# Performance work log

Measured on AMD Instinct MI355X. Metric: run time of the kernel, lower is better.

The kernel has to match this reference:

```python
import jax, jax.numpy as jnp
import numpy as np

DIM = 512
HEADS = 16
WIN = (8, 8)
N = WIN[0] * WIN[1]  # 64 tokens per window
BW = 1024            # batch * num_windows
TABLE = (2 * WIN[0] - 1) * (2 * WIN[1] - 1)  # 225


def _relative_position_index():
    ch, cw = np.arange(WIN[0]), np.arange(WIN[1])
    coords = np.stack(np.meshgrid(ch, cw, indexing='ij'))        # [2,Wh,Ww]
    flat = coords.reshape(2, -1)                                  # [2,N]
    rel = flat[:, :, None] - flat[:, None, :]                     # [2,N,N]
    rel = rel.transpose(1, 2, 0).astype(np.int64)                 # [N,N,2]
    rel[:, :, 0] += WIN[0] - 1
    rel[:, :, 1] += WIN[1] - 1
    rel[:, :, 0] *= 2 * WIN[1] - 1
    return jnp.asarray(rel.sum(-1), dtype=jnp.int32)              # [N,N]


def setup_inputs() -> dict:
    key = jax.random.key(0)
    ks = jax.random.split(key, 8)
    s = 0.02
    return {
        'q': jax.random.normal(ks[0], (BW, N, DIM), jnp.float32),
        'wq': jax.random.normal(ks[1], (DIM, DIM), jnp.float32) * s,
        'bq': jnp.zeros((DIM,), jnp.float32),
        'wkv': jax.random.normal(ks[2], (DIM, 2 * DIM), jnp.float32) * s,
        'bkv': jnp.zeros((2 * DIM,), jnp.float32),
        'wproj': jax.random.normal(ks[3], (DIM, DIM), jnp.float32) * s,
        'bproj': jnp.zeros((DIM,), jnp.float32),
        'bias_table': jax.random.normal(ks[4], (TABLE, HEADS), jnp.float32) * s,
        'rel_pos_index': _relative_position_index(),
    }


def reference(q, wq, bq, wkv, bkv, wproj, bproj, bias_table, rel_pos_index):
    B, n, C = q.shape
    hd = C // HEADS
    scale = hd ** -0.5
    # projections (torch Linear with pre-transposed weights)
    qh = (q @ wq + bq).reshape(B, n, HEADS, hd).transpose(0, 2, 1, 3) * scale  # [B,H,N,hd]
    kv = (q @ wkv + bkv).reshape(B, n, 2, HEADS, hd)
    k = kv[:, :, 0].transpose(0, 2, 1, 3)  # [B,H,N,hd]
    v = kv[:, :, 1].transpose(0, 2, 1, 3)
    attn = jnp.einsum('bhqd,bhkd->bhqk', qh, k)                   # [B,H,N,N]
    bias = bias_table[rel_pos_index].transpose(2, 0, 1)           # [H,N,N]
    attn = jax.nn.softmax(attn + bias[None], axis=-1)
    x = jnp.einsum('bhqk,bhkd->bqhd', attn, v).reshape(B, n, C)
    x = x @ wproj + bproj
    return x, attn
```

## Files before the change

kernel.cpp:

```cpp
#include <hip/hip_runtime.h>
#include <hip/hip_bf16.h>
#include <stdint.h>

typedef __attribute__((ext_vector_type(8))) __bf16 bf16x8;
typedef __attribute__((ext_vector_type(4))) float f32x4;

#define MFMA16(a, b, c) __builtin_amdgcn_mfma_f32_16x16x32_bf16(a, b, c, 0, 0, 0)

__device__ __forceinline__ void gload16(const void* g, void* l) {
  __builtin_amdgcn_global_load_lds((const __attribute__((address_space(1))) void*)g,
                                   (__attribute__((address_space(3))) void*)l, 16, 0, 0);
}

__global__ __launch_bounds__(256) void prep_kernel(
    const float* __restrict__ wq, const float* __restrict__ bq,
    const float* __restrict__ wkv, const float* __restrict__ bkv,
    const float* __restrict__ wproj, const float* __restrict__ btab,
    const int* __restrict__ relidx,
    __bf16* __restrict__ W1t, __bf16* __restrict__ WpT,
    float* __restrict__ bias1, float* __restrict__ bias_frag) {
  const float scale = 0.17677669529663687f;
  int t = blockIdx.x * 256 + threadIdx.x;
  if (t < 786432) {
    int j = t >> 9, kk = t & 511;
    float v = (j < 512) ? wq[kk * 512 + j] * scale : wkv[kk * 1024 + (j - 512)];
    W1t[t] = (__bf16)v;
  } else if (t < 1048576) {
    int u = t - 786432;
    int j = u >> 9, kk = u & 511;
    WpT[u] = (__bf16)wproj[kk * 512 + j];
  } else if (t < 1050112) {
    int j = t - 1048576;
    bias1[j] = (j < 512) ? bq[j] * scale : bkv[j - 512];
  } else if (t < 1115648) {
    int u = t - 1050112;
    int r = u & 3, l = (u >> 2) & 63, nj = (u >> 8) & 3, mi = (u >> 10) & 3, h = u >> 12;
    int qq = mi * 16 + (l >> 4) * 4 + r;
    int nn = nj * 16 + (l & 15);
    bias_frag[u] = btab[relidx[qq * 64 + nn] * 16 + h];
  }
}

__global__ __launch_bounds__(256) void cvt_kernel(const float* __restrict__ in,
                                                  __bf16* __restrict__ out) {
  int t = blockIdx.x * 256 + threadIdx.x;
  const float4* p = (const float4*)in + (size_t)t * 2;
  float4 a = p[0], b = p[1];
  bf16x8 v = {(__bf16)a.x, (__bf16)a.y, (__bf16)a.z, (__bf16)a.w,
              (__bf16)b.x, (__bf16)b.y, (__bf16)b.z, (__bf16)b.w};
  *((bf16x8*)out + t) = v;
}

__global__ __launch_bounds__(256) void gemm1_kernel(
    const __bf16* __restrict__ A, const __bf16* __restrict__ W1t,
    const float* __restrict__ bias1,
    __bf16* __restrict__ qh, __bf16* __restrict__ kb, __bf16* __restrict__ vv) {
  __shared__ __bf16 As[128 * 32];
  __shared__ __bf16 Bs[128 * 32];
  int tid = threadIdx.x;
  int w = tid >> 6, l = tid & 63, c = l & 15, g = l >> 4;
  int wm = w >> 1, wn = w & 1;
  int bflat = (blockIdx.x & 7) * 768 + (blockIdx.x >> 3);
  int bx = bflat % 12, by = bflat / 12;
  int r0 = by * 128, n0 = bx * 128;

  f32x4 acc[4][4] = {};
  int e0 = w * 1024 + l * 8;
  int rn0 = e0 >> 5, rk0 = e0 & 31;
  int e1 = e0 + 512;
  int rn1 = e1 >> 5, rk1 = e1 & 31;

  for (int kt = 0; kt < 16; ++kt) {
    int k0 = kt * 32;
    __syncthreads();
    gload16(A + (size_t)(r0 + rn0) * 512 + k0 + rk0, (void*)(As + w * 1024));
    gload16(A + (size_t)(r0 + rn1) * 512 + k0 + rk1, (void*)(As + w * 1024 + 512));
    gload16(W1t + (size_t)(n0 + rn0) * 512 + k0 + rk0, (void*)(Bs + w * 1024));
    gload16(W1t + (size_t)(n0 + rn1) * 512 + k0 + rk1, (void*)(Bs + w * 1024 + 512));
    __syncthreads();
    bf16x8 af[4], bfr[4];
#pragma unroll
    for (int mi = 0; mi < 4; mi++) af[mi] = *(const bf16x8*)(As + (wm * 64 + mi * 16 + c) * 32 + g * 8);
#pragma unroll
    for (int nj = 0; nj < 4; nj++) bfr[nj] = *(const bf16x8*)(Bs + (wn * 64 + nj * 16 + c) * 32 + g * 8);
#pragma unroll
    for (int mi = 0; mi < 4; mi++)
#pragma unroll
      for (int nj = 0; nj < 4; nj++)
        acc[mi][nj] = MFMA16(af[mi], bfr[nj], acc[mi][nj]);
  }

  __bf16* dst = (bx < 4) ? qh : (bx < 8) ? kb : vv;

  float bia[4];
#pragma unroll
  for (int nj = 0; nj < 4; nj++) bia[nj] = bias1[n0 + wn * 64 + nj * 16 + c];
  int rowbase = r0 + wm * 64 + g * 4;
  int colbase = n0 + wn * 64 + c;
#pragma unroll
  for (int mi = 0; mi < 4; mi++) {
#pragma unroll
    for (int nj = 0; nj < 4; nj++) {
      int col = colbase + nj * 16;
      int jj = col & 511;
      int h = jj >> 5, d = jj & 31;
#pragma unroll
      for (int r = 0; r < 4; r++) {
        int row = rowbase + mi * 16 + r;
        int b = row >> 6, tok = row & 63;
        float val = acc[mi][nj][r] + bia[nj];
        dst[(size_t)(b * 16 + h) * 2048 + tok * 32 + d] = (__bf16)val;
      }
    }
  }
}

__global__ __launch_bounds__(64) void attn_kernel(
    const __bf16* __restrict__ qh, const __bf16* __restrict__ kb,
    const __bf16* __restrict__ vv, const float* __restrict__ bias_frag,
    float* __restrict__ attn_out, __bf16* __restrict__ xpart) {
  __shared__ __bf16 P[64 * 72];
  __shared__ __bf16 Vlds[64 * 34];
  int bh = blockIdx.x;
  int b = bh >> 4, h = bh & 15;
  int l = threadIdx.x, c = l & 15, g = l >> 4;
  const __bf16* qp = qh + (size_t)bh * 2048;
  const __bf16* kp = kb + (size_t)bh * 2048;
  const __bf16* vp = vv + (size_t)bh * 2048;

  uint4 vst[4];
  const uint4* vg = (const uint4*)vp;
#pragma unroll
  for (int i = 0; i < 4; i++) vst[i] = vg[l + 64 * i];

  bf16x8 af[4], bfr[4];
#pragma unroll
  for (int mi = 0; mi < 4; mi++) af[mi] = *(const bf16x8*)(qp + (mi * 16 + c) * 32 + g * 8);
#pragma unroll
  for (int nj = 0; nj < 4; nj++) bfr[nj] = *(const bf16x8*)(kp + (nj * 16 + c) * 32 + g * 8);

  f32x4 acc[4][4];
#pragma unroll
  for (int mi = 0; mi < 4; mi++)
#pragma unroll
    for (int nj = 0; nj < 4; nj++)
      acc[mi][nj] = *(const f32x4*)(bias_frag + ((size_t)((h * 4 + mi) * 4 + nj) * 64 + l) * 4);

#pragma unroll
  for (int i = 0; i < 4; i++) {
    int ch = l + 64 * i;
    int row = ch >> 2, pos = ch & 3;
    uint32_t* pw = (uint32_t*)&Vlds[row * 34 + pos * 8];
    pw[0] = vst[i].x; pw[1] = vst[i].y; pw[2] = vst[i].z; pw[3] = vst[i].w;
  }

#pragma unroll
  for (int mi = 0; mi < 4; mi++)
#pragma unroll
    for (int nj = 0; nj < 4; nj++)
      acc[mi][nj] = MFMA16(af[mi], bfr[nj], acc[mi][nj]);

  float* ao = attn_out + (size_t)bh * 4096;
#pragma unroll
  for (int mi = 0; mi < 4; mi++) {
#pragma unroll
    for (int r = 0; r < 4; r++) {
      float m = fmaxf(fmaxf(acc[mi][0][r], acc[mi][1][r]), fmaxf(acc[mi][2][r], acc[mi][3][r]));
      m = fmaxf(m, __shfl_xor(m, 1));
      m = fmaxf(m, __shfl_xor(m, 2));
      m = fmaxf(m, __shfl_xor(m, 4));
      m = fmaxf(m, __shfl_xor(m, 8));
      float p0 = __expf(acc[mi][0][r] - m);
      float p1 = __expf(acc[mi][1][r] - m);
      float p2 = __expf(acc[mi][2][r] - m);
      float p3 = __expf(acc[mi][3][r] - m);
      float s = p0 + p1 + p2 + p3;
      s += __shfl_xor(s, 1);
      s += __shfl_xor(s, 2);
      s += __shfl_xor(s, 4);
      s += __shfl_xor(s, 8);
      float rs = 1.0f / s;
      p0 *= rs; p1 *= rs; p2 *= rs; p3 *= rs;
      int row = mi * 16 + g * 4 + r;
      ao[row * 64 + c] = p0;
      ao[row * 64 + 16 + c] = p1;
      ao[row * 64 + 32 + c] = p2;
      ao[row * 64 + 48 + c] = p3;
      P[row * 72 + c] = (__bf16)p0;
      P[row * 72 + 16 + c] = (__bf16)p1;
      P[row * 72 + 32 + c] = (__bf16)p2;
      P[row * 72 + 48 + c] = (__bf16)p3;
    }
  }
  __syncthreads();

  bf16x8 pa[4][2];
#pragma unroll
  for (int mi = 0; mi < 4; mi++)
#pragma unroll
    for (int kk = 0; kk < 2; kk++)
      pa[mi][kk] = *(const bf16x8*)(P + (mi * 16 + c) * 72 + kk * 32 + g * 8);

  bf16x8 bv[2][2];
#pragma unroll
  for (int dj = 0; dj < 2; dj++)
#pragma unroll
    for (int kk = 0; kk < 2; kk++)
#pragma unroll
      for (int e = 0; e < 8; e++)
        bv[dj][kk][e] = Vlds[(32 * kk + 8 * g + e) * 34 + 16 * dj + c];

  f32x4 xacc[4][2] = {};
#pragma unroll
  for (int mi = 0; mi < 4; mi++)
#pragma unroll
    for (int dj = 0; dj < 2; dj++)
#pragma unroll
      for (int kk = 0; kk < 2; kk++)
        xacc[mi][dj] = MFMA16(pa[mi][kk], bv[dj][kk], xacc[mi][dj]);

  __bf16* xp = xpart + (size_t)b * 64 * 512 + h * 32;
#pragma unroll
  for (int mi = 0; mi < 4; mi++)
#pragma unroll
    for (int dj = 0; dj < 2; dj++)
#pragma unroll
      for (int r = 0; r < 4; r++) {
        int row = mi * 16 + g * 4 + r;
        xp[(size_t)row * 512 + dj * 16 + c] = (__bf16)xacc[mi][dj][r];
      }
}

__global__ __launch_bounds__(256) void gemm2_kernel(
    const __bf16* __restrict__ A, const __bf16* __restrict__ WpT,
    const float* __restrict__ bproj, float* __restrict__ out) {
  __shared__ __bf16 As[128 * 32];
  __shared__ __bf16 Bs[128 * 32];
  int tid = threadIdx.x;
  int w = tid >> 6, l = tid & 63, c = l & 15, g = l >> 4;
  int wm = w >> 1, wn = w & 1;
  int bflat = (blockIdx.x & 7) * 256 + (blockIdx.x >> 3);
  int bx = bflat & 3, by = bflat >> 2;
  int r0 = by * 128, n0 = bx * 128;

  f32x4 acc[4][4] = {};
  int e0 = w * 1024 + l * 8;
  int rn0 = e0 >> 5, rk0 = e0 & 31;
  int e1 = e0 + 512;
  int rn1 = e1 >> 5, rk1 = e1 & 31;

  for (int kt = 0; kt < 16; ++kt) {
    int k0 = kt * 32;
    __syncthreads();
    gload16(A + (size_t)(r0 + rn0) * 512 + k0 + rk0, (void*)(As + w * 1024));
    gload16(A + (size_t)(r0 + rn1) * 512 + k0 + rk1, (void*)(As + w * 1024 + 512));
    gload16(WpT + (size_t)(n0 + rn0) * 512 + k0 + rk0, (void*)(Bs + w * 1024));
    gload16(WpT + (size_t)(n0 + rn1) * 512 + k0 + rk1, (void*)(Bs + w * 1024 + 512));
    __syncthreads();
    bf16x8 af[4], bfr[4];
#pragma unroll
    for (int mi = 0; mi < 4; mi++) af[mi] = *(const bf16x8*)(As + (wm * 64 + mi * 16 + c) * 32 + g * 8);
#pragma unroll
    for (int nj = 0; nj < 4; nj++) bfr[nj] = *(const bf16x8*)(Bs + (wn * 64 + nj * 16 + c) * 32 + g * 8);
#pragma unroll
    for (int mi = 0; mi < 4; mi++)
#pragma unroll
      for (int nj = 0; nj < 4; nj++)
        acc[mi][nj] = MFMA16(af[mi], bfr[nj], acc[mi][nj]);
  }

  float bia[4];
#pragma unroll
  for (int nj = 0; nj < 4; nj++) bia[nj] = bproj[n0 + wn * 64 + nj * 16 + c];
  int rowbase = r0 + wm * 64 + g * 4;
  int colbase = n0 + wn * 64 + c;
#pragma unroll
  for (int mi = 0; mi < 4; mi++)
#pragma unroll
    for (int nj = 0; nj < 4; nj++)
#pragma unroll
      for (int r = 0; r < 4; r++) {
        int row = rowbase + mi * 16 + r;
        out[(size_t)row * 512 + colbase + nj * 16] = acc[mi][nj][r] + bia[nj];
      }
}

extern "C" void kernel_launch(void* const* d_in, const int* in_sizes, int n_in,
                              void* d_out, int out_size, void* d_ws, size_t ws_size,
                              hipStream_t stream) {
  const float* q = (const float*)d_in[0];
  const float* wq = (const float*)d_in[1];
  const float* bq = (const float*)d_in[2];
  const float* wkv = (const float*)d_in[3];
  const float* bkv = (const float*)d_in[4];
  const float* wproj = (const float*)d_in[5];
  const float* bproj = (const float*)d_in[6];
  const float* btab = (const float*)d_in[7];
  const int* relidx = (const int*)d_in[8];

  float* x_out = (float*)d_out;
  float* attn_out = x_out + 33554432;
  __bf16* qbf = (__bf16*)attn_out;

  char* ws = (char*)d_ws;
  __bf16* qh = (__bf16*)(ws);
  __bf16* kb = (__bf16*)(ws + 67108864);
  __bf16* vv = (__bf16*)(ws + 134217728);
  __bf16* xpart = (__bf16*)(ws + 201326592);
  __bf16* W1t = (__bf16*)(ws + 268435456);
  __bf16* WpT = (__bf16*)(ws + 270008320);
  float* bias1 = (float*)(ws + 270532608);
  float* bfrag = (float*)(ws + 270538752);

  hipLaunchKernelGGL(prep_kernel, dim3(4358), dim3(256), 0, stream,
                     wq, bq, wkv, bkv, wproj, btab, relidx, W1t, WpT, bias1, bfrag);
  hipLaunchKernelGGL(cvt_kernel, dim3(16384), dim3(256), 0, stream, q, qbf);
  hipLaunchKernelGGL(gemm1_kernel, dim3(6144), dim3(256), 0, stream,
                     qbf, W1t, bias1, qh, kb, vv);
  hipLaunchKernelGGL(attn_kernel, dim3(16384), dim3(64), 0, stream,
                     qh, kb, vv, bfrag, attn_out, xpart);
  hipLaunchKernelGGL(gemm2_kernel, dim3(2048), dim3(256), 0, stream,
                     xpart, WpT, bproj, x_out);
}
```

Baseline: 801.5 us.

## Fuse attention with output projection and merge weight prep with input conversion

Attention and the output projection now run in one kernel. Each 512-thread block handles half a window (32 tokens) across all 16 heads, keeps the attention output in swizzled LDS, and multiplies it directly by WpT read from global memory. This removes the xpart round trip through HBM and one kernel launch. The weight-prep and input-conversion kernels are also merged into a single launch. In exchange, V is read from global memory with scalar strided loads, WpT is re-read per block without LDS staging, and there are fewer, larger blocks.

```diff
diff --git a/kernel.cpp b/kernel.cpp
--- a/kernel.cpp
+++ b/kernel.cpp
@@ -12,15 +12,25 @@
                                    (__attribute__((address_space(3))) void*)l, 16, 0, 0);
 }
 
-__global__ __launch_bounds__(256) void prep_kernel(
+__global__ __launch_bounds__(256) void prep_cvt_kernel(
+    const float* __restrict__ qin, __bf16* __restrict__ qbf,
     const float* __restrict__ wq, const float* __restrict__ bq,
     const float* __restrict__ wkv, const float* __restrict__ bkv,
     const float* __restrict__ wproj, const float* __restrict__ btab,
     const int* __restrict__ relidx,
     __bf16* __restrict__ W1t, __bf16* __restrict__ WpT,
     float* __restrict__ bias1, float* __restrict__ bias_frag) {
+  if (blockIdx.x < 16384) {
+    int t = blockIdx.x * 256 + threadIdx.x;
+    const float4* p = (const float4*)qin + (size_t)t * 2;
+    float4 a = p[0], b = p[1];
+    bf16x8 v = {(__bf16)a.x, (__bf16)a.y, (__bf16)a.z, (__bf16)a.w,
+                (__bf16)b.x, (__bf16)b.y, (__bf16)b.z, (__bf16)b.w};
+    *((bf16x8*)qbf + t) = v;
+    return;
+  }
   const float scale = 0.17677669529663687f;
-  int t = blockIdx.x * 256 + threadIdx.x;
+  int t = (blockIdx.x - 16384) * 256 + threadIdx.x;
   if (t < 786432) {
     int j = t >> 9, kk = t & 511;
     float v = (j < 512) ? wq[kk * 512 + j] * scale : wkv[kk * 1024 + (j - 512)];
@@ -41,16 +51,6 @@
   }
 }
 
-__global__ __launch_bounds__(256) void cvt_kernel(const float* __restrict__ in,
-                                                  __bf16* __restrict__ out) {
-  int t = blockIdx.x * 256 + threadIdx.x;
-  const float4* p = (const float4*)in + (size_t)t * 2;
-  float4 a = p[0], b = p[1];
-  bf16x8 v = {(__bf16)a.x, (__bf16)a.y, (__bf16)a.z, (__bf16)a.w,
-              (__bf16)b.x, (__bf16)b.y, (__bf16)b.z, (__bf16)b.w};
-  *((bf16x8*)out + t) = v;
-}
-
 __global__ __launch_bounds__(256) void gemm1_kernel(
     const __bf16* __restrict__ A, const __bf16* __restrict__ W1t,
     const float* __restrict__ bias1,
@@ -115,173 +115,143 @@
   }
 }
 
-__global__ __launch_bounds__(64) void attn_kernel(
+__global__ __launch_bounds__(512) void attn_proj_kernel(
     const __bf16* __restrict__ qh, const __bf16* __restrict__ kb,
     const __bf16* __restrict__ vv, const float* __restrict__ bias_frag,
-    float* __restrict__ attn_out, __bf16* __restrict__ xpart) {
-  __shared__ __bf16 P[64 * 72];
-  __shared__ __bf16 Vlds[64 * 34];
-  int bh = blockIdx.x;
-  int b = bh >> 4, h = bh & 15;
-  int l = threadIdx.x, c = l & 15, g = l >> 4;
-  const __bf16* qp = qh + (size_t)bh * 2048;
-  const __bf16* kp = kb + (size_t)bh * 2048;
-  const __bf16* vp = vv + (size_t)bh * 2048;
-
-  uint4 vst[4];
-  const uint4* vg = (const uint4*)vp;
-#pragma unroll
-  for (int i = 0; i < 4; i++) vst[i] = vg[l + 64 * i];
-
-  bf16x8 af[4], bfr[4];
-#pragma unroll
-  for (int mi = 0; mi < 4; mi++) af[mi] = *(const bf16x8*)(qp + (mi * 16 + c) * 32 + g * 8);
-#pragma unroll
-  for (int nj = 0; nj < 4; nj++) bfr[nj] = *(const bf16x8*)(kp + (nj * 16 + c) * 32 + g * 8);
-
-  f32x4 acc[4][4];
-#pragma unroll
-  for (int mi = 0; mi < 4; mi++)
-#pragma unroll
-    for (int nj = 0; nj < 4; nj++)
-      acc[mi][nj] = *(const f32x4*)(bias_frag + ((size_t)((h * 4 + mi) * 4 + nj) * 64 + l) * 4);
-
-#pragma unroll
-  for (int i = 0; i < 4; i++) {
-    int ch = l + 64 * i;
-    int row = ch >> 2, pos = ch & 3;
-    uint32_t* pw = (uint32_t*)&Vlds[row * 34 + pos * 8];
-    pw[0] = vst[i].x; pw[1] = vst[i].y; pw[2] = vst[i].z; pw[3] = vst[i].w;
-  }
-
-#pragma unroll
-  for (int mi = 0; mi < 4; mi++)
-#pragma unroll
-    for (int nj = 0; nj < 4; nj++)
-      acc[mi][nj] = MFMA16(af[mi], bfr[nj], acc[mi][nj]);
-
-  float* ao = attn_out + (size_t)bh * 4096;
-#pragma unroll
-  for (int mi = 0; mi < 4; mi++) {
-#pragma unroll
-    for (int r = 0; r < 4; r++) {
-      float m = fmaxf(fmaxf(acc[mi][0][r], acc[mi][1][r]), fmaxf(acc[mi][2][r], acc[mi][3][r]));
-      m = fmaxf(m, __shfl_xor(m, 1));
-      m = fmaxf(m, __shfl_xor(m, 2));
-      m = fmaxf(m, __shfl_xor(m, 4));
-      m = fmaxf(m, __shfl_xor(m, 8));
-      float p0 = __expf(acc[mi][0][r] - m);
-      float p1 = __expf(acc[mi][1][r] - m);
-      float p2 = __expf(acc[mi][2][r] - m);
-      float p3 = __expf(acc[mi][3][r] - m);
-      float s = p0 + p1 + p2 + p3;
-      s += __shfl_xor(s, 1);
-      s += __shfl_xor(s, 2);
-      s += __shfl_xor(s, 4);
-      s += __shfl_xor(s, 8);
-      float rs = 1.0f / s;
-      p0 *= rs; p1 *= rs; p2 *= rs; p3 *= rs;
-      int row = mi * 16 + g * 4 + r;
-      ao[row * 64 + c] = p0;
-      ao[row * 64 + 16 + c] = p1;
-      ao[row * 64 + 32 + c] = p2;
-      ao[row * 64 + 48 + c] = p3;
-      P[row * 72 + c] = (__bf16)p0;
-      P[row * 72 + 16 + c] = (__bf16)p1;
-      P[row * 72 + 32 + c] = (__bf16)p2;
-      P[row * 72 + 48 + c] = (__bf16)p3;
-    }
-  }
-  __syncthreads();
-
-  bf16x8 pa[4][2];
-#pragma unroll
-  for (int mi = 0; mi < 4; mi++)
-#pragma unroll
-    for (int kk = 0; kk < 2; kk++)
-      pa[mi][kk] = *(const bf16x8*)(P + (mi * 16 + c) * 72 + kk * 32 + g * 8);
-
-  bf16x8 bv[2][2];
-#pragma unroll
-  for (int dj = 0; dj < 2; dj++)
-#pragma unroll
-    for (int kk = 0; kk < 2; kk++)
-#pragma unroll
-      for (int e = 0; e < 8; e++)
-        bv[dj][kk][e] = Vlds[(32 * kk + 8 * g + e) * 34 + 16 * dj + c];
-
-  f32x4 xacc[4][2] = {};
-#pragma unroll
-  for (int mi = 0; mi < 4; mi++)
-#pragma unroll
-    for (int dj = 0; dj < 2; dj++)
-#pragma unroll
-      for (int kk = 0; kk < 2; kk++)
-        xacc[mi][dj] = MFMA16(pa[mi][kk], bv[dj][kk], xacc[mi][dj]);
-
-  __bf16* xp = xpart + (size_t)b * 64 * 512 + h * 32;
-#pragma unroll
-  for (int mi = 0; mi < 4; mi++)
-#pragma unroll
-    for (int dj = 0; dj < 2; dj++)
-#pragma unroll
-      for (int r = 0; r < 4; r++) {
-        int row = mi * 16 + g * 4 + r;
-        xp[(size_t)row * 512 + dj * 16 + c] = (__bf16)xacc[mi][dj][r];
-      }
-}
-
-__global__ __launch_bounds__(256) void gemm2_kernel(
-    const __bf16* __restrict__ A, const __bf16* __restrict__ WpT,
-    const float* __restrict__ bproj, float* __restrict__ out) {
-  __shared__ __bf16 As[128 * 32];
-  __shared__ __bf16 Bs[128 * 32];
+    const __bf16* __restrict__ WpT, const float* __restrict__ bproj,
+    float* __restrict__ attn_out, float* __restrict__ x_out) {
+  __shared__ __align__(16) __bf16 Pb[8][16 * 76];
+  __shared__ __align__(16) char xinb[32 * 1024];
+  int bid = blockIdx.x;
+  int b = bid >> 1, half = bid & 1, tok0 = half * 32;
   int tid = threadIdx.x;
   int w = tid >> 6, l = tid & 63, c = l & 15, g = l >> 4;
-  int wm = w >> 1, wn = w & 1;
-  int bflat = (blockIdx.x & 7) * 256 + (blockIdx.x >> 3);
-  int bx = bflat & 3, by = bflat >> 2;
-  int r0 = by * 128, n0 = bx * 128;
-
-  f32x4 acc[4][4] = {};
-  int e0 = w * 1024 + l * 8;
-  int rn0 = e0 >> 5, rk0 = e0 & 31;
-  int e1 = e0 + 512;
-  int rn1 = e1 >> 5, rk1 = e1 & 31;
-
+  __bf16* pb = &Pb[w][0];
+
+#pragma unroll
+  for (int hi = 0; hi < 2; ++hi) {
+    int h = w * 2 + hi;
+    int bh = b * 16 + h;
+    const __bf16* qp = qh + (size_t)bh * 2048;
+    const __bf16* kp = kb + (size_t)bh * 2048;
+    const __bf16* vp = vv + (size_t)bh * 2048;
+
+    bf16x8 bv[2][2];
+#pragma unroll
+    for (int dj = 0; dj < 2; dj++)
+#pragma unroll
+      for (int kk = 0; kk < 2; kk++)
+#pragma unroll
+        for (int e = 0; e < 8; e++)
+          bv[dj][kk][e] = vp[(32 * kk + 8 * g + e) * 32 + 16 * dj + c];
+
+    bf16x8 af[2], bfr[4];
+#pragma unroll
+    for (int mi = 0; mi < 2; mi++) af[mi] = *(const bf16x8*)(qp + (tok0 + mi * 16 + c) * 32 + g * 8);
+#pragma unroll
+    for (int nj = 0; nj < 4; nj++) bfr[nj] = *(const bf16x8*)(kp + (nj * 16 + c) * 32 + g * 8);
+
+    f32x4 acc[2][4];
+#pragma unroll
+    for (int mi = 0; mi < 2; mi++)
+#pragma unroll
+      for (int nj = 0; nj < 4; nj++)
+        acc[mi][nj] = *(const f32x4*)(bias_frag +
+            ((size_t)((h * 4 + half * 2 + mi) * 4 + nj) * 64 + l) * 4);
+#pragma unroll
+    for (int mi = 0; mi < 2; mi++)
+#pragma unroll
+      for (int nj = 0; nj < 4; nj++)
+        acc[mi][nj] = MFMA16(af[mi], bfr[nj], acc[mi][nj]);
+
+    float* ao = attn_out + (size_t)bh * 4096;
+    f32x4 xacc[2][2] = {};
+#pragma unroll
+    for (int mi = 0; mi < 2; mi++) {
+#pragma unroll
+      for (int r = 0; r < 4; r++) {
+        float m = fmaxf(fmaxf(acc[mi][0][r], acc[mi][1][r]), fmaxf(acc[mi][2][r], acc[mi][3][r]));
+        m = fmaxf(m, __shfl_xor(m, 1));
+        m = fmaxf(m, __shfl_xor(m, 2));
+        m = fmaxf(m, __shfl_xor(m, 4));
+        m = fmaxf(m, __shfl_xor(m, 8));
+        float p0 = __expf(acc[mi][0][r] - m);
+        float p1 = __expf(acc[mi][1][r] - m);
+        float p2 = __expf(acc[mi][2][r] - m);
+        float p3 = __expf(acc[mi][3][r] - m);
+        float s = p0 + p1 + p2 + p3;
+        s += __shfl_xor(s, 1);
+        s += __shfl_xor(s, 2);
+        s += __shfl_xor(s, 4);
+        s += __shfl_xor(s, 8);
+        float rs = 1.0f / s;
+        p0 *= rs; p1 *= rs; p2 *= rs; p3 *= rs;
+        int rl = g * 4 + r;
+        int rowg = tok0 + mi * 16 + rl;
+        ao[rowg * 64 + c] = p0;
+        ao[rowg * 64 + 16 + c] = p1;
+        ao[rowg * 64 + 32 + c] = p2;
+        ao[rowg * 64 + 48 + c] = p3;
+        pb[rl * 76 + c] = (__bf16)p0;
+        pb[rl * 76 + 16 + c] = (__bf16)p1;
+        pb[rl * 76 + 32 + c] = (__bf16)p2;
+        pb[rl * 76 + 48 + c] = (__bf16)p3;
+      }
+      bf16x8 pa[2];
+#pragma unroll
+      for (int kk = 0; kk < 2; kk++)
+        pa[kk] = *(const bf16x8*)(pb + c * 76 + kk * 32 + g * 8);
+#pragma unroll
+      for (int dj = 0; dj < 2; dj++)
+#pragma unroll
+        for (int kk = 0; kk < 2; kk++)
+          xacc[mi][dj] = MFMA16(pa[kk], bv[dj][kk], xacc[mi][dj]);
+    }
+
+#pragma unroll
+    for (int mi = 0; mi < 2; mi++)
+#pragma unroll
+      for (int dj = 0; dj < 2; dj++)
+#pragma unroll
+        for (int r = 0; r < 4; r++) {
+          int row = mi * 16 + g * 4 + r;
+          int col = h * 32 + dj * 16 + c;
+          int byte = (row * 1024 + col * 2) ^ ((row & 7) << 4);
+          *(__bf16*)(xinb + byte) = (__bf16)xacc[mi][dj][r];
+        }
+  }
+  __syncthreads();
+
+  int n0 = w * 64;
+  f32x4 acc2[2][4] = {};
   for (int kt = 0; kt < 16; ++kt) {
-    int k0 = kt * 32;
-    __syncthreads();
-    gload16(A + (size_t)(r0 + rn0) * 512 + k0 + rk0, (void*)(As + w * 1024));
-    gload16(A + (size_t)(r0 + rn1) * 512 + k0 + rk1, (void*)(As + w * 1024 + 512));
-    gload16(WpT + (size_t)(n0 + rn0) * 512 + k0 + rk0, (void*)(Bs + w * 1024));
-    gload16(WpT + (size_t)(n0 + rn1) * 512 + k0 + rk1, (void*)(Bs + w * 1024 + 512));
-    __syncthreads();
-    bf16x8 af[4], bfr[4];
-#pragma unroll
-    for (int mi = 0; mi < 4; mi++) af[mi] = *(const bf16x8*)(As + (wm * 64 + mi * 16 + c) * 32 + g * 8);
-#pragma unroll
-    for (int nj = 0; nj < 4; nj++) bfr[nj] = *(const bf16x8*)(Bs + (wn * 64 + nj * 16 + c) * 32 + g * 8);
-#pragma unroll
-    for (int mi = 0; mi < 4; mi++)
-#pragma unroll
-      for (int nj = 0; nj < 4; nj++)
-        acc[mi][nj] = MFMA16(af[mi], bfr[nj], acc[mi][nj]);
-  }
-
+    bf16x8 af2[2], bfr2[4];
+#pragma unroll
+    for (int mi = 0; mi < 2; mi++) {
+      int row = mi * 16 + c;
+      int byte = (row * 1024 + kt * 64 + g * 16) ^ ((row & 7) << 4);
+      af2[mi] = *(const bf16x8*)(xinb + byte);
+    }
+#pragma unroll
+    for (int nj = 0; nj < 4; nj++)
+      bfr2[nj] = *(const bf16x8*)(WpT + (size_t)(n0 + nj * 16 + c) * 512 + kt * 32 + g * 8);
+#pragma unroll
+    for (int mi = 0; mi < 2; mi++)
+#pragma unroll
+      for (int nj = 0; nj < 4; nj++)
+        acc2[mi][nj] = MFMA16(af2[mi], bfr2[nj], acc2[mi][nj]);
+  }
   float bia[4];
 #pragma unroll
-  for (int nj = 0; nj < 4; nj++) bia[nj] = bproj[n0 + wn * 64 + nj * 16 + c];
-  int rowbase = r0 + wm * 64 + g * 4;
-  int colbase = n0 + wn * 64 + c;
-#pragma unroll
-  for (int mi = 0; mi < 4; mi++)
+  for (int nj = 0; nj < 4; nj++) bia[nj] = bproj[n0 + nj * 16 + c];
+#pragma unroll
+  for (int mi = 0; mi < 2; mi++)
 #pragma unroll
     for (int nj = 0; nj < 4; nj++)
 #pragma unroll
       for (int r = 0; r < 4; r++) {
-        int row = rowbase + mi * 16 + r;
-        out[(size_t)row * 512 + colbase + nj * 16] = acc[mi][nj][r] + bia[nj];
+        int row = b * 64 + tok0 + mi * 16 + g * 4 + r;
+        x_out[(size_t)row * 512 + n0 + nj * 16 + c] = acc2[mi][nj][r] + bia[nj];
       }
 }
 
@@ -306,19 +276,15 @@
   __bf16* qh = (__bf16*)(ws);
   __bf16* kb = (__bf16*)(ws + 67108864);
   __bf16* vv = (__bf16*)(ws + 134217728);
-  __bf16* xpart = (__bf16*)(ws + 201326592);
-  __bf16* W1t = (__bf16*)(ws + 268435456);
-  __bf16* WpT = (__bf16*)(ws + 270008320);
-  float* bias1 = (float*)(ws + 270532608);
-  float* bfrag = (float*)(ws + 270538752);
-
-  hipLaunchKernelGGL(prep_kernel, dim3(4358), dim3(256), 0, stream,
-                     wq, bq, wkv, bkv, wproj, btab, relidx, W1t, WpT, bias1, bfrag);
-  hipLaunchKernelGGL(cvt_kernel, dim3(16384), dim3(256), 0, stream, q, qbf);
+  __bf16* W1t = (__bf16*)(ws + 201326592);
+  __bf16* WpT = (__bf16*)(ws + 202899456);
+  float* bias1 = (float*)(ws + 203423744);
+  float* bfrag = (float*)(ws + 203429888);
+
+  hipLaunchKernelGGL(prep_cvt_kernel, dim3(20742), dim3(256), 0, stream,
+                     q, qbf, wq, bq, wkv, bkv, wproj, btab, relidx, W1t, WpT, bias1, bfrag);
   hipLaunchKernelGGL(gemm1_kernel, dim3(6144), dim3(256), 0, stream,
                      qbf, W1t, bias1, qh, kb, vv);
-  hipLaunchKernelGGL(attn_kernel, dim3(16384), dim3(64), 0, stream,
-                     qh, kb, vv, bfrag, attn_out, xpart);
-  hipLaunchKernelGGL(gemm2_kernel, dim3(2048), dim3(256), 0, stream,
-                     xpart, WpT, bproj, x_out);
-}
+  hipLaunchKernelGGL(attn_proj_kernel, dim3(2048), dim3(512), 0, stream,
+                     qh, kb, vv, bfrag, WpT, bproj, attn_out, x_out);
+}
```

Result: slower. 826.2 us (+3.1%).
